# Optimization experiments

Measured on AMD Instinct MI355X. Metric: run time of the kernel, lower is better.

Reference implementation:

```python
import jax, jax.numpy as jnp
import numpy as np

B, L, H, E = 2, 2048, 16, 64

def setup_inputs() -> dict:
    key = jax.random.key(0)
    kq, kk, kv = jax.random.split(key, 3)
    queries = jax.random.normal(kq, (B, L, H, E), dtype=jnp.float32)
    keys = jax.random.normal(kk, (B, L, H, E), dtype=jnp.float32)
    values = jax.random.normal(kv, (B, L, H, E), dtype=jnp.float32)
    # causal mask: True above the diagonal gets masked out (as in torch.triu(..., diagonal=1))
    attn_mask = jnp.broadcast_to(
        jnp.triu(jnp.ones((L, L), dtype=bool), k=1)[None, None, :, :], (B, 1, L, L)
    )
    return {"queries": queries, "keys": keys, "values": values, "attn_mask": attn_mask}

def reference(queries, keys, values, attn_mask):
    Ef = queries.shape[-1]
    # scores: [B, H, L, S]
    scores = jnp.einsum('blhe,bshe->bhls', queries, keys)
    scores = jnp.where(attn_mask, -jnp.inf, scores)
    # FAITHFUL to source: scale = 1/sqrt(E), then scores * (1.0/scale) = scores * sqrt(E)
    scale = 1.0 / jnp.sqrt(jnp.float32(Ef))
    attention_weights = jax.nn.softmax(scores * (1.0 / scale), axis=-1)
    # dropout p = 0.0 -> identity
    V = jnp.einsum('bhls,bshe->blhe', attention_weights, values)
    return V
```

## Files before the change

### kernel.cpp

```cpp
#include <hip/hip_runtime.h>

#define Bb 2
#define Ls 2048
#define Hh 16
#define Ee 64

#define QT 128
#define KT 64
#define BUFB 24576

typedef __fp16 f16;
typedef __attribute__((ext_vector_type(2))) __fp16 f16x2;
typedef __attribute__((ext_vector_type(8))) __fp16 f16x8;
typedef __attribute__((ext_vector_type(4))) float  f32x4;

union Frag  { f16x8 v; f16x2 h[4]; unsigned int u[4]; };
union U32H2 { f16x2 h; unsigned int u; };

__device__ __forceinline__ f16x2 pkrtz(float a, float b) {
  return __builtin_amdgcn_cvt_pkrtz(a, b);
}
__device__ __forceinline__ f32x4 mfma16(f16x8 a, f16x8 b, f32x4 c) {
  return __builtin_amdgcn_mfma_f32_16x16x32_f16(a, b, c, 0, 0, 0);
}

#define SC 11.541560327111707f

__launch_bounds__(512, 4)
__global__ void fattn(const float* __restrict__ Q, const float* __restrict__ K,
                      const float* __restrict__ V, float* __restrict__ O) {
  __shared__ __align__(16) char lds[2 * BUFB];

  const int tid  = threadIdx.x;
  const int lane = tid & 63;
  const int wid  = tid >> 6;
  const int g    = lane >> 4;
  const int q15  = lane & 15;
  const int bid  = blockIdx.x;

  const int bh  = bid & 31;
  const int qtx = bid >> 5;
  const int qt  = (qtx < 8) ? qtx : 23 - qtx;
  const int b   = bh >> 4;
  const int h   = bh & 15;

  const int q0   = qt * QT;
  const int q0w  = q0 + wid * 16;
  const int qrow = q0w + q15;

  f16x8 qh[2], ql[2];
  {
    const float* qp = Q + (((size_t)(b * Ls + qrow) * Hh) + h) * Ee + 8 * g;
#pragma unroll
    for (int c = 0; c < 2; ++c) {
      float x[8];
      *(float4*)&x[0] = *(const float4*)(qp + 32 * c);
      *(float4*)&x[4] = *(const float4*)(qp + 32 * c + 4);
      Frag fh, fl;
#pragma unroll
      for (int j = 0; j < 4; ++j) {
        f16x2 hi = pkrtz(x[2 * j], x[2 * j + 1]);
        fl.h[j] = pkrtz(x[2 * j] - (float)hi[0], x[2 * j + 1] - (float)hi[1]);
        fh.h[j] = hi;
      }
      qh[c] = fh.v;
      ql[c] = fl.v;
    }
  }

  const int r    = tid >> 3;
  const int cbe  = (tid & 7) * 8;
  const int kv0  = (tid & 31) * 2;
  const int ec4  = (tid >> 5) * 4;
  const float* kp0 = K + (((size_t)(b * Ls + r) * Hh) + h) * Ee + cbe;
  const float* vp0 = V + (((size_t)(b * Ls + kv0) * Hh) + h) * Ee + ec4;
  const int rowstride = Hh * Ee;

  float4 ka0, ka1, va0, vb0;

#define STAGE_LOAD(KB)                                          \
  {                                                             \
    const float* kp = kp0 + (size_t)(KB) * rowstride;           \
    ka0 = *(const float4*)(kp);                                 \
    ka1 = *(const float4*)(kp + 4);                             \
    const float* vp = vp0 + (size_t)(KB) * rowstride;           \
    va0 = *(const float4*)(vp);                                 \
    vb0 = *(const float4*)(vp + rowstride);                     \
  }

#define STAGE_WRITE(BUF)                                        \
  {                                                             \
    char* Khi = (BUF);                                          \
    char* Klo = (BUF) + 8192;                                   \
    char* Vt  = (BUF) + 16384;                                  \
    float x[8];                                                 \
    *(float4*)&x[0] = ka0; *(float4*)&x[4] = ka1;               \
    Frag fh, fl;                                                \
    _Pragma("unroll")                                           \
    for (int j = 0; j < 4; ++j) {                               \
      f16x2 hi = pkrtz(x[2 * j], x[2 * j + 1]);                 \
      fl.h[j] = pkrtz(x[2 * j] - (float)hi[0],                  \
                      x[2 * j + 1] - (float)hi[1]);             \
      fh.h[j] = hi;                                             \
    }                                                           \
    const int sw = (r & 7) << 4;                                \
    *(f16x8*)(Khi + r * 128 + ((cbe * 2) ^ sw)) = fh.v;         \
    *(f16x8*)(Klo + r * 128 + ((cbe * 2) ^ sw)) = fl.v;         \
    _Pragma("unroll")                                           \
    for (int j = 0; j < 4; ++j) {                               \
      U32H2 pr;                                                 \
      pr.h = pkrtz(va0[j], vb0[j]);                             \
      const int e = ec4 + j;                                    \
      *(unsigned int*)(Vt + e * 128 + ((kv0 * 2) ^ ((e & 7) << 4))) = pr.u; \
    }                                                           \
  }

  f32x4 o0, o1, o2, o3;
#pragma unroll
  for (int i = 0; i < 4; ++i) { o0[i] = 0.f; o1[i] = 0.f; o2[i] = 0.f; o3[i] = 0.f; }
  float m = -3.0e38f, l = 0.f;

  const int NT = 2 * (qt + 1);

  STAGE_LOAD(0);
  STAGE_WRITE(lds);
  __syncthreads();
  int cur = 0;

  const int swr   = (q15 & 7) << 4;
  const int srcA  = q15 + ((g & 1) ? 32 : 0);
  const int srcB  = srcA + 16;
  const int srel  = g >> 1;
  const int lbase = lane & 48;

  for (int t = 0; t < NT; ++t) {
    const int kb = t * KT;
    const bool pf = (t + 1 < NT);
    if (pf) STAGE_LOAD(kb + KT);

    if (kb <= q0w + 15) {
      char* bufc = lds + cur * BUFB;
      char* Khi = bufc;
      char* Klo = bufc + 8192;
      char* Vt  = bufc + 16384;

      f32x4 p4[4];
      __builtin_amdgcn_s_setprio(1);
#pragma unroll
      for (int st = 0; st < 4; ++st) {
        const char* kh = Khi + (16 * st + q15) * 128;
        const char* kl = Klo + (16 * st + q15) * 128;
        f32x4 acch, accl;
#pragma unroll
        for (int i = 0; i < 4; ++i) { acch[i] = 0.f; accl[i] = 0.f; }
#pragma unroll
        for (int c = 0; c < 2; ++c) {
          const int off = ((c << 6) + (g << 4)) ^ swr;
          f16x8 ah = *(const f16x8*)(kh + off);
          f16x8 al = *(const f16x8*)(kl + off);
          acch = mfma16(ah, qh[c], acch);
          accl = mfma16(ah, ql[c], accl);
          accl = mfma16(al, qh[c], accl);
        }
        p4[st] = acch + accl;
      }
      __builtin_amdgcn_s_setprio(0);

      if (kb + KT - 1 > q0w) {
#pragma unroll
        for (int st = 0; st < 4; ++st)
#pragma unroll
          for (int rg = 0; rg < 4; ++rg) {
            const int kv = kb + 16 * st + 4 * g + rg;
            if (kv > qrow) p4[st][rg] = -3.0e38f;
          }
      }

      f32x4 tv = p4[0];
#pragma unroll
      for (int i = 0; i < 4; ++i) tv[i] = fmaxf(fmaxf(p4[0][i], p4[1][i]), fmaxf(p4[2][i], p4[3][i]));
      float tm = fmaxf(fmaxf(tv[0], tv[1]), fmaxf(tv[2], tv[3]));
      tm = fmaxf(tm, __shfl_xor(tm, 16));
      tm = fmaxf(tm, __shfl_xor(tm, 32));

      if (__any(tm > m + 1.0f)) {
        const float mnew = fmaxf(m, tm);
        const float corr = __builtin_amdgcn_exp2f((m - mnew) * SC);
        l *= corr;
#pragma unroll
        for (int rg = 0; rg < 4; ++rg) {
          const float cr = __shfl(corr, lbase | (4 * g + rg));
          o0[rg] *= cr; o1[rg] *= cr; o2[rg] *= cr; o3[rg] *= cr;
        }
        m = mnew;
      }
      const float base = m * SC;
#pragma unroll
      for (int st = 0; st < 4; ++st)
#pragma unroll
        for (int rg = 0; rg < 4; ++rg)
          p4[st][rg] = __builtin_amdgcn_exp2f(p4[st][rg] * SC - base);

      {
        f32x4 sv = (p4[0] + p4[1]) + (p4[2] + p4[3]);
        float ps = (sv[0] + sv[1]) + (sv[2] + sv[3]);
        ps += __shfl_xor(ps, 16);
        ps += __shfl_xor(ps, 32);
        l += ps;
      }

      unsigned int u[8];
#pragma unroll
      for (int st = 0; st < 4; ++st) {
        U32H2 w0, w1;
        w0.h = pkrtz(p4[st][0], p4[st][1]);
        w1.h = pkrtz(p4[st][2], p4[st][3]);
        u[2 * st]     = w0.u;
        u[2 * st + 1] = w1.u;
      }
      f16x8 pa[2];
#pragma unroll
      for (int c = 0; c < 2; ++c) {
        const unsigned a0 = (unsigned)__shfl((int)u[4 * c + 0], srcA);
        const unsigned a1 = (unsigned)__shfl((int)u[4 * c + 1], srcA);
        const unsigned a2 = (unsigned)__shfl((int)u[4 * c + 0], srcB);
        const unsigned a3 = (unsigned)__shfl((int)u[4 * c + 1], srcB);
        const unsigned b0 = (unsigned)__shfl((int)u[4 * c + 2], srcA);
        const unsigned b1 = (unsigned)__shfl((int)u[4 * c + 3], srcA);
        const unsigned b2 = (unsigned)__shfl((int)u[4 * c + 2], srcB);
        const unsigned b3 = (unsigned)__shfl((int)u[4 * c + 3], srcB);
        Frag f;
        f.u[0] = srel ? b0 : a0;
        f.u[1] = srel ? b1 : a1;
        f.u[2] = srel ? b2 : a2;
        f.u[3] = srel ? b3 : a3;
        pa[c] = f.v;
      }

      __builtin_amdgcn_s_setprio(1);
#pragma unroll
      for (int c = 0; c < 2; ++c) {
        const int coff = ((c << 6) + (g << 4)) ^ swr;
        const f16x8 v0 = *(const f16x8*)(Vt + (q15)      * 128 + coff);
        const f16x8 v1 = *(const f16x8*)(Vt + (16 + q15) * 128 + coff);
        const f16x8 v2 = *(const f16x8*)(Vt + (32 + q15) * 128 + coff);
        const f16x8 v3 = *(const f16x8*)(Vt + (48 + q15) * 128 + coff);
        o0 = mfma16(pa[c], v0, o0);
        o1 = mfma16(pa[c], v1, o1);
        o2 = mfma16(pa[c], v2, o2);
        o3 = mfma16(pa[c], v3, o3);
      }
      __builtin_amdgcn_s_setprio(0);
    }

    if (pf) STAGE_WRITE(lds + (cur ^ 1) * BUFB);
    __syncthreads();
    cur ^= 1;
  }

  const float inv = 1.0f / l;
#pragma unroll
  for (int rg = 0; rg < 4; ++rg) {
    const float iv = __shfl(inv, lbase | (4 * g + rg));
    float* op = O + (((size_t)(b * Ls + q0w + 4 * g + rg) * Hh) + h) * Ee + q15;
    op[0]  = o0[rg] * iv;
    op[16] = o1[rg] * iv;
    op[32] = o2[rg] * iv;
    op[48] = o3[rg] * iv;
  }
}

extern "C" void kernel_launch(void* const* d_in, const int* in_sizes, int n_in,
                              void* d_out, int out_size, void* d_ws, size_t ws_size,
                              hipStream_t stream) {
  const float* Q = (const float*)d_in[0];
  const float* K = (const float*)d_in[1];
  const float* V = (const float*)d_in[2];
  float* O = (float*)d_out;
  (void)in_sizes; (void)n_in; (void)out_size; (void)d_ws; (void)ws_size;
  fattn<<<dim3(Bb * Hh * (Ls / QT)), dim3(512), 0, stream>>>(Q, K, V, O);
}
```

Measured before the change: 164.3 us.

## Halve query tile to 64 rows with 256-thread blocks and heaviest-first ordering

Shrinks the query tile from 128 to 64 rows and the block from 512 to 256 threads, which doubles the grid to 1024 blocks. Blocks are ordered so the largest causal tiles launch first, replacing the earlier paired folding scheme. Each thread now stages twice as many K/V elements per tile, and the per-wave skip of fully masked KV tiles is dropped because it is no longer needed. The aim is finer load balance and more blocks in flight, at the cost of re-reading K/V more often per query row and fewer waves sharing each staged tile.

```diff
diff --git a/kernel.cpp b/kernel.cpp
--- a/kernel.cpp
+++ b/kernel.cpp
@@ -5,7 +5,7 @@
 #define Hh 16
 #define Ee 64
 
-#define QT 128
+#define QT 64
 #define KT 64
 #define BUFB 24576
 
@@ -26,7 +26,7 @@
 
 #define SC 11.541560327111707f
 
-__launch_bounds__(512, 4)
+__launch_bounds__(256, 3)
 __global__ void fattn(const float* __restrict__ Q, const float* __restrict__ K,
                       const float* __restrict__ V, float* __restrict__ O) {
   __shared__ __align__(16) char lds[2 * BUFB];
@@ -39,8 +39,7 @@
   const int bid  = blockIdx.x;
 
   const int bh  = bid & 31;
-  const int qtx = bid >> 5;
-  const int qt  = (qtx < 8) ? qtx : 23 - qtx;
+  const int qt  = 31 - (bid >> 5);
   const int b   = bh >> 4;
   const int h   = bh & 15;
 
@@ -68,51 +67,67 @@
     }
   }
 
-  const int r    = tid >> 3;
-  const int cbe  = (tid & 7) * 8;
+  const int r    = tid >> 2;
+  const int cbe  = (tid & 3) * 16;
   const int kv0  = (tid & 31) * 2;
-  const int ec4  = (tid >> 5) * 4;
+  const int ec   = tid >> 5;
   const float* kp0 = K + (((size_t)(b * Ls + r) * Hh) + h) * Ee + cbe;
-  const float* vp0 = V + (((size_t)(b * Ls + kv0) * Hh) + h) * Ee + ec4;
+  const float* vp0 = V + (((size_t)(b * Ls + kv0) * Hh) + h) * Ee + ec * 8;
   const int rowstride = Hh * Ee;
 
-  float4 ka0, ka1, va0, vb0;
-
-#define STAGE_LOAD(KB)                                          \
-  {                                                             \
-    const float* kp = kp0 + (size_t)(KB) * rowstride;           \
-    ka0 = *(const float4*)(kp);                                 \
-    ka1 = *(const float4*)(kp + 4);                             \
-    const float* vp = vp0 + (size_t)(KB) * rowstride;           \
-    va0 = *(const float4*)(vp);                                 \
-    vb0 = *(const float4*)(vp + rowstride);                     \
-  }
-
-#define STAGE_WRITE(BUF)                                        \
-  {                                                             \
-    char* Khi = (BUF);                                          \
-    char* Klo = (BUF) + 8192;                                   \
-    char* Vt  = (BUF) + 16384;                                  \
-    float x[8];                                                 \
-    *(float4*)&x[0] = ka0; *(float4*)&x[4] = ka1;               \
-    Frag fh, fl;                                                \
-    _Pragma("unroll")                                           \
-    for (int j = 0; j < 4; ++j) {                               \
-      f16x2 hi = pkrtz(x[2 * j], x[2 * j + 1]);                 \
-      fl.h[j] = pkrtz(x[2 * j] - (float)hi[0],                  \
-                      x[2 * j + 1] - (float)hi[1]);             \
-      fh.h[j] = hi;                                             \
-    }                                                           \
-    const int sw = (r & 7) << 4;                                \
-    *(f16x8*)(Khi + r * 128 + ((cbe * 2) ^ sw)) = fh.v;         \
-    *(f16x8*)(Klo + r * 128 + ((cbe * 2) ^ sw)) = fl.v;         \
-    _Pragma("unroll")                                           \
-    for (int j = 0; j < 4; ++j) {                               \
-      U32H2 pr;                                                 \
-      pr.h = pkrtz(va0[j], vb0[j]);                             \
-      const int e = ec4 + j;                                    \
+  float4 ka0, ka1, ka2, ka3, va0, va1, vb0, vb1;
+
+#define STAGE_LOAD(KB)                                              \
+  {                                                                 \
+    const float* kp = kp0 + (size_t)(KB) * rowstride;               \
+    ka0 = *(const float4*)(kp);                                     \
+    ka1 = *(const float4*)(kp + 4);                                 \
+    ka2 = *(const float4*)(kp + 8);                                 \
+    ka3 = *(const float4*)(kp + 12);                                \
+    const float* vp = vp0 + (size_t)(KB) * rowstride;               \
+    va0 = *(const float4*)(vp);                                     \
+    va1 = *(const float4*)(vp + 4);                                 \
+    vb0 = *(const float4*)(vp + rowstride);                         \
+    vb1 = *(const float4*)(vp + rowstride + 4);                     \
+  }
+
+#define STAGE_WRITE(BUF)                                            \
+  {                                                                 \
+    char* Khi = (BUF);                                              \
+    char* Klo = (BUF) + 8192;                                       \
+    char* Vt  = (BUF) + 16384;                                      \
+    float x[16];                                                    \
+    *(float4*)&x[0]  = ka0; *(float4*)&x[4]  = ka1;                 \
+    *(float4*)&x[8]  = ka2; *(float4*)&x[12] = ka3;                 \
+    Frag fh0, fl0, fh1, fl1;                                        \
+    _Pragma("unroll")                                               \
+    for (int j = 0; j < 4; ++j) {                                   \
+      f16x2 hi0 = pkrtz(x[2 * j], x[2 * j + 1]);                    \
+      fl0.h[j] = pkrtz(x[2 * j] - (float)hi0[0],                    \
+                       x[2 * j + 1] - (float)hi0[1]);               \
+      fh0.h[j] = hi0;                                               \
+      f16x2 hi1 = pkrtz(x[8 + 2 * j], x[8 + 2 * j + 1]);            \
+      fl1.h[j] = pkrtz(x[8 + 2 * j] - (float)hi1[0],                \
+                       x[8 + 2 * j + 1] - (float)hi1[1]);           \
+      fh1.h[j] = hi1;                                               \
+    }                                                               \
+    const int sw = (r & 7) << 4;                                    \
+    char* dh = Khi + r * 128;                                       \
+    char* dl = Klo + r * 128;                                       \
+    *(f16x8*)(dh + ((cbe * 2) ^ sw))      = fh0.v;                  \
+    *(f16x8*)(dh + ((cbe * 2 + 16) ^ sw)) = fh1.v;                  \
+    *(f16x8*)(dl + ((cbe * 2) ^ sw))      = fl0.v;                  \
+    *(f16x8*)(dl + ((cbe * 2 + 16) ^ sw)) = fl1.v;                  \
+    float y0[8], y1[8];                                             \
+    *(float4*)&y0[0] = va0; *(float4*)&y0[4] = va1;                 \
+    *(float4*)&y1[0] = vb0; *(float4*)&y1[4] = vb1;                 \
+    _Pragma("unroll")                                               \
+    for (int j = 0; j < 8; ++j) {                                   \
+      U32H2 pr;                                                     \
+      pr.h = pkrtz(y0[j], y1[j]);                                   \
+      const int e = ec * 8 + j;                                     \
       *(unsigned int*)(Vt + e * 128 + ((kv0 * 2) ^ ((e & 7) << 4))) = pr.u; \
-    }                                                           \
+    }                                                               \
   }
 
   f32x4 o0, o1, o2, o3;
@@ -120,7 +135,7 @@
   for (int i = 0; i < 4; ++i) { o0[i] = 0.f; o1[i] = 0.f; o2[i] = 0.f; o3[i] = 0.f; }
   float m = -3.0e38f, l = 0.f;
 
-  const int NT = 2 * (qt + 1);
+  const int NT = qt + 1;
 
   STAGE_LOAD(0);
   STAGE_WRITE(lds);
@@ -138,7 +153,7 @@
     const bool pf = (t + 1 < NT);
     if (pf) STAGE_LOAD(kb + KT);
 
-    if (kb <= q0w + 15) {
+    {
       char* bufc = lds + cur * BUFB;
       char* Khi = bufc;
       char* Klo = bufc + 8192;
@@ -176,7 +191,7 @@
           }
       }
 
-      f32x4 tv = p4[0];
+      f32x4 tv;
 #pragma unroll
       for (int i = 0; i < 4; ++i) tv[i] = fmaxf(fmaxf(p4[0][i], p4[1][i]), fmaxf(p4[2][i], p4[3][i]));
       float tm = fmaxf(fmaxf(tv[0], tv[1]), fmaxf(tv[2], tv[3]));
@@ -278,5 +293,5 @@
   const float* V = (const float*)d_in[2];
   float* O = (float*)d_out;
   (void)in_sizes; (void)n_in; (void)out_size; (void)d_ws; (void)ws_size;
-  fattn<<<dim3(Bb * Hh * (Ls / QT)), dim3(512), 0, stream>>>(Q, K, V, O);
-}
+  fattn<<<dim3(Bb * Hh * (Ls / QT)), dim3(256), 0, stream>>>(Q, K, V, O);
+}
```

Measured after the change: 163.2 us. No clear change (-0.7%).
